# Kernel tuning notes

Measured on AMD Instinct MI355X. Metric: run time of the kernel, lower is better.

The kernel has to match this reference:

```python
import jax, jax.numpy as jnp
import numpy as np

NUM_HEADS = 16


def setup_inputs() -> dict:
    key = jax.random.key(0)
    ks = jax.random.split(key, 7)
    B, S, D = 2, 2048, 1024
    scale = 1.0 / np.sqrt(D)
    return {
        "queries": jax.random.normal(ks[0], (B, S, D), jnp.float32),
        "keys": jax.random.normal(ks[1], (B, S, D), jnp.float32),
        "values": jax.random.normal(ks[2], (B, S, D), jnp.float32),
        "Wq": jax.random.normal(ks[3], (D, D), jnp.float32) * scale,
        "Wk": jax.random.normal(ks[4], (D, D), jnp.float32) * scale,
        "Wv": jax.random.normal(ks[5], (D, D), jnp.float32) * scale,
        "Wo": jax.random.normal(ks[6], (D, D), jnp.float32) * scale,
    }


def _split_heads(x, h):
    # [B, S, D] -> [B, h, S, D/h]
    B, S, D = x.shape
    return x.reshape(B, S, h, D // h).transpose(0, 2, 1, 3)


def reference(queries, keys, values, Wq, Wk, Wv, Wo):
    h = NUM_HEADS
    q = _split_heads(queries @ Wq, h)  # [B, h, S, dh]
    k = _split_heads(keys @ Wk, h)
    v = _split_heads(values @ Wv, h)
    dh = q.shape[-1]
    scores = jnp.einsum("bhqd,bhkd->bhqk", q, k) / jnp.sqrt(jnp.float32(dh))
    attn = jax.nn.softmax(scores, axis=-1)
    y = jnp.einsum("bhqk,bhkd->bhqd", attn, v)  # [B, h, S, dh]
    B, _, S, _ = y.shape
    y = y.transpose(0, 2, 1, 3).reshape(B, S, h * dh)
    return y @ Wo
```

## Files before the change

kernel.cpp:

```cpp
#include <hip/hip_runtime.h>
#include <hip/hip_bf16.h>


typedef __attribute__((ext_vector_type(8))) short bf16x8;
typedef __attribute__((ext_vector_type(4))) float f32x4;
typedef __attribute__((ext_vector_type(16))) float f32x16;
typedef __attribute__((ext_vector_type(4))) unsigned int u32x4;

#define QSCALE 0.18033688011112042f

__device__ __forceinline__ unsigned short f2b(float f) {
    unsigned int u = __float_as_uint(f);
    u += 0x7FFFu + ((u >> 16) & 1u);
    return (unsigned short)(u >> 16);
}

__device__ __forceinline__ unsigned cvt_pk_bf16(float lo, float hi) {
    unsigned r;
    asm("v_cvt_pk_bf16_f32 %0, %1, %2" : "=v"(r) : "v"(lo), "v"(hi));
    return r;
}

__device__ __forceinline__ void gld_lds16(const void* g, void* l) {
    __builtin_amdgcn_global_load_lds(
        (const __attribute__((address_space(1))) unsigned int*)g,
        (__attribute__((address_space(3))) unsigned int*)l, 16, 0, 0);
}

__global__ __launch_bounds__(256) void f32_to_bf16_3(
    const float* __restrict__ i0, const float* __restrict__ i1, const float* __restrict__ i2,
    unsigned short* __restrict__ o0, unsigned short* __restrict__ o1, unsigned short* __restrict__ o2)
{
    const int z = blockIdx.y;
    const float* in = z == 0 ? i0 : (z == 1 ? i1 : i2);
    unsigned short* out = z == 0 ? o0 : (z == 1 ? o1 : o2);
    int i = blockIdx.x * 256 + threadIdx.x;
    float4 v = ((const float4*)in)[i];
    ushort4 o;
    o.x = f2b(v.x); o.y = f2b(v.y); o.z = f2b(v.z); o.w = f2b(v.w);
    ((ushort4*)out)[i] = o;
}

__global__ __launch_bounds__(256) void transpose_w4(
    const float* __restrict__ W0, const float* __restrict__ W1,
    const float* __restrict__ W2, const float* __restrict__ W3,
    unsigned short* __restrict__ O0, unsigned short* __restrict__ O1,
    unsigned short* __restrict__ O2, unsigned short* __restrict__ O3)
{
    __shared__ unsigned short tile[32][33];
    const int z = blockIdx.z;
    const float* in = z == 0 ? W0 : z == 1 ? W1 : z == 2 ? W2 : W3;
    unsigned short* out = z == 0 ? O0 : z == 1 ? O1 : z == 2 ? O2 : O3;
    const int c0 = blockIdx.x * 32, r0 = blockIdx.y * 32;
    const int tx = threadIdx.x, ty = threadIdx.y;
#pragma unroll
    for (int i = 0; i < 4; ++i)
        tile[ty + i * 8][tx] = f2b(in[(size_t)(r0 + ty + i * 8) * 1024 + c0 + tx]);
    __syncthreads();
#pragma unroll
    for (int i = 0; i < 4; ++i)
        out[(size_t)(c0 + ty + i * 8) * 1024 + r0 + tx] = tile[tx][ty + i * 8];
}

__device__ __forceinline__ void vpack_store(unsigned short* Vp, int gr, int gc,
                                            const f32x4& a)
{
    int bq = gr >> 11, kvg = gr & 2047, kvt = kvg >> 6;
    int h = gc >> 6, d = gc & 63;
    size_t img = ((size_t)(bq * 16 + h) * 32 + kvt) * 4096;
    int kvb = kvg & 63;
    int T = kvb >> 5, g = (kvb >> 3) & 3, hib = (kvb >> 2) & 1;
    int kstep = 2 * T + (g >> 1);
    int dt = d >> 5, ln31 = d & 31;
    size_t addr = img + dt * 2048 + kstep * 512 + hib * 256 + ln31 * 8 + (g & 1) * 4;
    uint2 w;
    w.x = cvt_pk_bf16(a[0], a[1]);
    w.y = cvt_pk_bf16(a[2], a[3]);
    *(uint2*)(Vp + addr) = w;
}

__device__ __forceinline__ int lds_fragaddr(int slot, int mat, int half, int row,
                                            int ks, int lg)
{
    int c8s = lg ^ ((row >> 1) & 3);
    return slot * 32768 + mat * 16384 + half * 8192 +
           (((row >> 4) * 2 + ks) * 512) + (row & 15) * 32 + c8s * 8;
}

__global__ __launch_bounds__(512, 2) void gemm256(
    const unsigned short* __restrict__ A0, const unsigned short* __restrict__ A1,
    const unsigned short* __restrict__ A2,
    const unsigned short* __restrict__ B0, const unsigned short* __restrict__ B1,
    const unsigned short* __restrict__ B2,
    unsigned short* __restrict__ Cq,
    unsigned short* __restrict__ Ckrm,
    unsigned short* __restrict__ Cv)
{
    __shared__ unsigned short lds[65536];
    const int tid = threadIdx.x;
    const int wid = tid >> 6, ln = tid & 15, lg = (tid & 63) >> 4;
    const int wr = wid >> 2, wc = wid & 3;
    const int z = blockIdx.z;
    const unsigned short* A = (z == 0) ? A0 : (z == 1) ? A1 : A2;
    const unsigned short* Bt = (z == 0) ? B0 : (z == 1) ? B1 : B2;
    const int m0 = blockIdx.y * 256, n0 = blockIdx.x * 256;

    f32x4 acc[8][4];
#pragma unroll
    for (int m = 0; m < 8; ++m)
#pragma unroll
        for (int n = 0; n < 4; ++n) acc[m][n] = {};

    const unsigned short* srcA[2][2];
    const unsigned short* srcB[2][2];
#pragma unroll
    for (int j = 0; j < 2; ++j) {
        const int ci = tid + j * 512;
        const int s = ci >> 6, r16 = (ci >> 2) & 15, c8 = ci & 3;
        const int c8s = c8 ^ ((r16 >> 1) & 3);
        const int rih = (s >> 1) * 16 + r16;
        const int colc = (s & 1) * 4 + c8s;
#pragma unroll
        for (int half = 0; half < 2; ++half) {
            srcA[j][half] = A + (size_t)(m0 + half * 128 + rih) * 1024 + colc * 8;
            srcB[j][half] = Bt + (size_t)(n0 + half * 128 + rih) * 1024 + colc * 8;
        }
    }

    auto stage = [&](int slot, int k0) {
#pragma unroll
        for (int j = 0; j < 2; ++j) {
            const int ci = tid + j * 512;
#pragma unroll
            for (int half = 0; half < 2; ++half) {
                gld_lds16(srcA[j][half] + k0,
                          &lds[slot * 32768 + half * 8192 + ci * 8]);
                gld_lds16(srcB[j][half] + k0,
                          &lds[slot * 32768 + 16384 + half * 8192 + ci * 8]);
            }
        }
    };

    stage(0, 0);
    __syncthreads();

    for (int t = 0; t < 16; ++t) {
        const int slot = t & 1;
        if (t < 15) stage(slot ^ 1, (t + 1) * 64);

#pragma unroll
        for (int qd = 0; qd < 4; ++qd) {
            const int mh = qd >> 1, nh = qd & 1;
            bf16x8 af[4][2], bfr[2][2];
#pragma unroll
            for (int mm = 0; mm < 4; ++mm)
#pragma unroll
                for (int ks = 0; ks < 2; ++ks)
                    af[mm][ks] = *(const bf16x8*)&lds[
                        lds_fragaddr(slot, 0, wr, (mh * 4 + mm) * 16 + ln, ks, lg)];
#pragma unroll
            for (int nn = 0; nn < 2; ++nn)
#pragma unroll
                for (int ks = 0; ks < 2; ++ks)
                    bfr[nn][ks] = *(const bf16x8*)&lds[
                        lds_fragaddr(slot, 1, wc >> 1,
                                     (wc & 1) * 64 + (nh * 2 + nn) * 16 + ln, ks, lg)];
            __builtin_amdgcn_s_setprio(1);
#pragma unroll
            for (int mm = 0; mm < 4; ++mm)
#pragma unroll
                for (int nn = 0; nn < 2; ++nn)
#pragma unroll
                    for (int ks = 0; ks < 2; ++ks)
                        acc[mh * 4 + mm][nh * 2 + nn] =
                            __builtin_amdgcn_mfma_f32_16x16x32_bf16(
                                af[mm][ks], bfr[nn][ks],
                                acc[mh * 4 + mm][nh * 2 + nn], 0, 0, 0);
            __builtin_amdgcn_s_setprio(0);
        }
        __syncthreads();
    }

#pragma unroll
    for (int m = 0; m < 8; ++m)
#pragma unroll
        for (int n = 0; n < 4; ++n) {
            const int gr = m0 + wr * 128 + m * 16 + lg * 4;
            const int gc = n0 + wc * 64 + n * 16 + ln;
            if (z == 0) {
#pragma unroll
                for (int r = 0; r < 4; ++r)
                    Cq[(size_t)(gr + r) * 1024 + gc] = f2b(acc[m][n][r] * QSCALE);
            } else if (z == 1) {
#pragma unroll
                for (int r = 0; r < 4; ++r)
                    Ckrm[(size_t)(gr + r) * 1024 + gc] = f2b(acc[m][n][r]);
            } else {
                vpack_store(Cv, gr, gc, acc[m][n]);
            }
        }
}

template <int BN, int MODE>
__global__ __launch_bounds__(256) void gemm_bt(
    const unsigned short* __restrict__ A0,
    const unsigned short* __restrict__ B0,
    void* __restrict__ Cq)
{
    constexpr int K = 1024, N = 1024;
    constexpr int NB = BN / 32;
    __shared__ unsigned short lds_a[2][128 * 32];
    __shared__ unsigned short lds_b[2][BN * 32];
    const int tid = threadIdx.x;
    const int wid = tid >> 6, ln = tid & 15, lg = (tid & 63) >> 4;
    const unsigned short* A = A0;
    const unsigned short* Bt = B0;
    const int m0 = blockIdx.y * 128, n0 = blockIdx.x * BN;
    const int wr = wid >> 1, wc = wid & 1;

    f32x4 acc[4][NB];
#pragma unroll
    for (int m = 0; m < 4; ++m)
#pragma unroll
        for (int n = 0; n < NB; ++n) acc[m][n] = {};

    const unsigned short* ga = A + (size_t)(m0 + (tid >> 2)) * K + (tid & 3) * 8;
    const unsigned short* gb = Bt + (size_t)(n0 + (tid >> 2)) * K + (tid & 3) * 8;

    auto stage = [&](int buf, int k0) {
        gld_lds16(ga + k0, &lds_a[buf][wid * 512]);
        gld_lds16(ga + k0 + 64 * K, &lds_a[buf][wid * 512 + 2048]);
        gld_lds16(gb + k0, &lds_b[buf][wid * 512]);
        if constexpr (BN == 128) gld_lds16(gb + k0 + 64 * K, &lds_b[buf][wid * 512 + 2048]);
    };

    stage(0, 0);
    __syncthreads();

    for (int k0 = 0; k0 < K; k0 += 32) {
        const int buf = (k0 >> 5) & 1;
        if (k0 + 32 < K) stage(buf ^ 1, k0 + 32);

        bf16x8 af[4], bfr[NB];
#pragma unroll
        for (int m = 0; m < 4; ++m)
            af[m] = *(const bf16x8*)&lds_a[buf][(wr * 64 + m * 16 + ln) * 32 + lg * 8];
#pragma unroll
        for (int n = 0; n < NB; ++n)
            bfr[n] = *(const bf16x8*)&lds_b[buf][(wc * (BN / 2) + n * 16 + ln) * 32 + lg * 8];
#pragma unroll
        for (int m = 0; m < 4; ++m)
#pragma unroll
            for (int n = 0; n < NB; ++n)
                acc[m][n] = __builtin_amdgcn_mfma_f32_16x16x32_bf16(af[m], bfr[n], acc[m][n], 0, 0, 0);
        __syncthreads();
    }

    const int gcb = n0 + wc * (BN / 2) + ln;
    const int grb = m0 + wr * 64 + lg * 4;
    float* C = (float*)Cq;
#pragma unroll
    for (int m = 0; m < 4; ++m)
#pragma unroll
        for (int n = 0; n < NB; ++n)
#pragma unroll
            for (int r = 0; r < 4; ++r)
                C[(size_t)(grb + m * 16 + r) * N + gcb + n * 16] = acc[m][n][r];
}

__global__ __launch_bounds__(256) void k_repack(
    const unsigned short* __restrict__ Krm, unsigned short* __restrict__ Kp)
{
    const int kvt = blockIdx.x, bh = blockIdx.y;
    const int bq = bh >> 4, h = bh & 15;
    const int tid = threadIdx.x;
    const int kvr = tid & 31, hib = (tid >> 5) & 1, ks = (tid >> 6) & 3;
    const size_t img = ((size_t)bh * 32 + kvt) * 4096;
#pragma unroll
    for (int T = 0; T < 2; ++T) {
        const int row = bq * 2048 + kvt * 64 + T * 32 + kvr;
        bf16x8 v = *(const bf16x8*)&Krm[(size_t)row * 1024 + h * 64 + ks * 16 + hib * 8];
        *(bf16x8*)&Kp[img + T * 2048 + ks * 512 + hib * 256 + kvr * 8] = v;
    }
}

__global__ __launch_bounds__(256) void attn_kernel(
    const unsigned short* __restrict__ Qp,
    const unsigned short* __restrict__ Kpack,
    const unsigned short* __restrict__ Vpack,
    unsigned short* __restrict__ Y)
{
    __shared__ unsigned short lds_k[2][4096];
    __shared__ unsigned short lds_v[2][4096];
    const int tid = threadIdx.x;
    const int wid = tid >> 6, lane = tid & 63;
    const int q31 = lane & 31, hi = lane >> 5;

    const int logical = (blockIdx.x & 7) * 64 + (blockIdx.x >> 3);
    const int bx = logical & 15, bh = logical >> 4;
    const int b = bh >> 4, h = bh & 15;
    const int tok0 = b * 2048;
    const int qw = bx * 128 + wid * 32;

    const unsigned short* qrow = Qp + (size_t)(tok0 + qw + q31) * 1024 + h * 64 + hi * 8;
    bf16x8 qf[4];
#pragma unroll
    for (int ks = 0; ks < 4; ++ks) qf[ks] = *(const bf16x8*)(qrow + ks * 16);

    const unsigned short* gk = Kpack + (size_t)bh * (32 * 4096);
    const unsigned short* gv = Vpack + (size_t)bh * (32 * 4096);

    float l_run = 0.f;
    f32x16 o[2] = {{}, {}};

    auto stage = [&](int buf, int kvt) {
#pragma unroll
        for (int j = 0; j < 2; ++j) {
            int seg = wid * 2 + j;
            gld_lds16(gk + (size_t)kvt * 4096 + seg * 512 + lane * 8, &lds_k[buf][seg * 512]);
            gld_lds16(gv + (size_t)kvt * 4096 + seg * 512 + lane * 8, &lds_v[buf][seg * 512]);
        }
    };

    stage(0, 0);
    __syncthreads();

    for (int kvt = 0; kvt < 32; ++kvt) {
        const int buf = kvt & 1;
        if (kvt < 31) stage(buf ^ 1, kvt + 1);

        f32x16 st[2];
#pragma unroll
        for (int T = 0; T < 2; ++T) {
            f32x16 zacc = {};
#pragma unroll
            for (int ks = 0; ks < 4; ++ks) {
                bf16x8 ka = *(const bf16x8*)&lds_k[buf][T * 2048 + ks * 512 + lane * 8];
                zacc = __builtin_amdgcn_mfma_f32_32x32x16_bf16(ka, qf[ks], zacc, 0, 0, 0);
            }
            st[T] = zacc;
        }

        float rs = 0.f;
        unsigned pk[2][8];
#pragma unroll
        for (int T = 0; T < 2; ++T)
#pragma unroll
            for (int g = 0; g < 4; ++g) {
                float p0 = __builtin_amdgcn_exp2f(st[T][g * 4 + 0]);
                float p1 = __builtin_amdgcn_exp2f(st[T][g * 4 + 1]);
                float p2 = __builtin_amdgcn_exp2f(st[T][g * 4 + 2]);
                float p3 = __builtin_amdgcn_exp2f(st[T][g * 4 + 3]);
                rs += (p0 + p1) + (p2 + p3);
                pk[T][g * 2 + 0] = cvt_pk_bf16(p0, p1);
                pk[T][g * 2 + 1] = cvt_pk_bf16(p2, p3);
            }
        rs += __shfl_xor(rs, 32);
        l_run += rs;

#pragma unroll
        for (int dt = 0; dt < 2; ++dt)
#pragma unroll
            for (int kstep = 0; kstep < 4; ++kstep) {
                bf16x8 va = *(const bf16x8*)&lds_v[buf][dt * 2048 + kstep * 512 + lane * 8];
                u32x4 w = {pk[kstep >> 1][4 * (kstep & 1) + 0], pk[kstep >> 1][4 * (kstep & 1) + 1],
                           pk[kstep >> 1][4 * (kstep & 1) + 2], pk[kstep >> 1][4 * (kstep & 1) + 3]};
                o[dt] = __builtin_amdgcn_mfma_f32_32x32x16_bf16(
                    va, __builtin_bit_cast(bf16x8, w), o[dt], 0, 0, 0);
            }
        __syncthreads();
    }

    const float inv = __builtin_amdgcn_rcpf(l_run);
    unsigned short* yout = Y + (size_t)(tok0 + qw + q31) * 1024 + h * 64 + hi * 4;
#pragma unroll
    for (int dt = 0; dt < 2; ++dt)
#pragma unroll
        for (int g = 0; g < 4; ++g) {
            uint2 w;
            w.x = cvt_pk_bf16(o[dt][g * 4 + 0] * inv, o[dt][g * 4 + 1] * inv);
            w.y = cvt_pk_bf16(o[dt][g * 4 + 2] * inv, o[dt][g * 4 + 3] * inv);
            *(uint2*)(yout + dt * 32 + g * 8) = w;
        }
}

extern "C" void kernel_launch(void* const* d_in, const int* in_sizes, int n_in,
                              void* d_out, int out_size, void* d_ws, size_t ws_size,
                              hipStream_t stream)
{
    const float* q_f = (const float*)d_in[0];
    const float* k_f = (const float*)d_in[1];
    const float* v_f = (const float*)d_in[2];
    const float* Wq  = (const float*)d_in[3];
    const float* Wk  = (const float*)d_in[4];
    const float* Wv  = (const float*)d_in[5];
    const float* Wo  = (const float*)d_in[6];
    float* out = (float*)d_out;

    const size_t X = (size_t)4096 * 1024;
    const size_t W = (size_t)1024 * 1024;
    unsigned short* ws  = (unsigned short*)d_ws;
    unsigned short* qb  = ws;
    unsigned short* kb  = qb + X;
    unsigned short* vb  = kb + X;
    unsigned short* wqt = vb + X;
    unsigned short* wkt = wqt + W;
    unsigned short* wvt = wkt + W;
    unsigned short* wot = wvt + W;
    unsigned short* Qp  = wot + W;
    unsigned short* Kpk = Qp + X;
    unsigned short* Vpk = Kpk + X;
    unsigned short* Yb  = Vpk + X;
    unsigned short* Krm = Yb;

    f32_to_bf16_3<<<dim3(4096, 3), 256, 0, stream>>>(q_f, k_f, v_f, qb, kb, vb);
    transpose_w4<<<dim3(32, 32, 4), dim3(32, 8), 0, stream>>>(Wq, Wk, Wv, Wo,
                                                              wqt, wkt, wvt, wot);

    gemm256<<<dim3(4, 16, 3), 512, 0, stream>>>(qb, kb, vb, wqt, wkt, wvt,
                                                Qp, Krm, Vpk);
    k_repack<<<dim3(32, 32), 256, 0, stream>>>(Krm, Kpk);

    attn_kernel<<<512, 256, 0, stream>>>(Qp, Kpk, Vpk, Yb);

    gemm_bt<64, 0><<<dim3(16, 32), 256, 0, stream>>>(Yb, wot, out);
}
```

Measured before the change: 221.8 us.

## Fuse K repack into projection GEMM epilogue and halve attention block size

The K projection GEMM now writes directly into the packed per-head tile layout used by attention, which removes the separate k_repack kernel and its extra read and write of the K matrix. The attention kernel goes from 256 to 128 threads per block and from 512 to 1024 blocks, each covering 64 queries, so each wave stages twice as many K/V segments. The fused store writes scalar bf16 values with a strided pattern, which may coalesce worse than the old row-major writes. Smaller blocks give more blocks for the scheduler but reuse each staged K/V tile across fewer query waves.

After: 231.0 us. 1.04x slower.

```diff
diff --git a/kernel.cpp b/kernel.cpp
--- a/kernel.cpp
+++ b/kernel.cpp
@@ -79,6 +79,20 @@
     *(uint2*)(Vp + addr) = w;
 }
 
+__device__ __forceinline__ void kpack_store(unsigned short* Kp, int gr0, int gc,
+                                            const f32x4& a)
+{
+    int bq = gr0 >> 11, kvg = gr0 & 2047, kvt = kvg >> 6;
+    int h = gc >> 6, d = gc & 63;
+    size_t img = ((size_t)(bq * 16 + h) * 32 + kvt) * 4096;
+    int ks = d >> 4, hib = (d >> 3) & 1, i = d & 7;
+    int kvb = kvg & 63, T = kvb >> 5;
+    size_t base = img + T * 2048 + ks * 512 + hib * 256 + i;
+#pragma unroll
+    for (int r = 0; r < 4; ++r)
+        Kp[base + ((kvb & 31) + r) * 8] = f2b(a[r]);
+}
+
 __device__ __forceinline__ int lds_fragaddr(int slot, int mat, int half, int row,
                                             int ks, int lg)
 {
@@ -93,7 +107,7 @@
     const unsigned short* __restrict__ B0, const unsigned short* __restrict__ B1,
     const unsigned short* __restrict__ B2,
     unsigned short* __restrict__ Cq,
-    unsigned short* __restrict__ Ckrm,
+    unsigned short* __restrict__ Ck,
     unsigned short* __restrict__ Cv)
 {
     __shared__ unsigned short lds[65536];
@@ -192,9 +206,7 @@
                 for (int r = 0; r < 4; ++r)
                     Cq[(size_t)(gr + r) * 1024 + gc] = f2b(acc[m][n][r] * QSCALE);
             } else if (z == 1) {
-#pragma unroll
-                for (int r = 0; r < 4; ++r)
-                    Ckrm[(size_t)(gr + r) * 1024 + gc] = f2b(acc[m][n][r]);
+                kpack_store(Ck, gr, gc, acc[m][n]);
             } else {
                 vpack_store(Cv, gr, gc, acc[m][n]);
             }
@@ -268,23 +280,7 @@
                 C[(size_t)(grb + m * 16 + r) * N + gcb + n * 16] = acc[m][n][r];
 }
 
-__global__ __launch_bounds__(256) void k_repack(
-    const unsigned short* __restrict__ Krm, unsigned short* __restrict__ Kp)
-{
-    const int kvt = blockIdx.x, bh = blockIdx.y;
-    const int bq = bh >> 4, h = bh & 15;
-    const int tid = threadIdx.x;
-    const int kvr = tid & 31, hib = (tid >> 5) & 1, ks = (tid >> 6) & 3;
-    const size_t img = ((size_t)bh * 32 + kvt) * 4096;
-#pragma unroll
-    for (int T = 0; T < 2; ++T) {
-        const int row = bq * 2048 + kvt * 64 + T * 32 + kvr;
-        bf16x8 v = *(const bf16x8*)&Krm[(size_t)row * 1024 + h * 64 + ks * 16 + hib * 8];
-        *(bf16x8*)&Kp[img + T * 2048 + ks * 512 + hib * 256 + kvr * 8] = v;
-    }
-}
-
-__global__ __launch_bounds__(256) void attn_kernel(
+__global__ __launch_bounds__(128) void attn_kernel(
     const unsigned short* __restrict__ Qp,
     const unsigned short* __restrict__ Kpack,
     const unsigned short* __restrict__ Vpack,
@@ -296,11 +292,11 @@
     const int wid = tid >> 6, lane = tid & 63;
     const int q31 = lane & 31, hi = lane >> 5;
 
-    const int logical = (blockIdx.x & 7) * 64 + (blockIdx.x >> 3);
-    const int bx = logical & 15, bh = logical >> 4;
+    const int logical = (blockIdx.x & 7) * 128 + (blockIdx.x >> 3);
+    const int bx = logical & 31, bh = logical >> 5;
     const int b = bh >> 4, h = bh & 15;
     const int tok0 = b * 2048;
-    const int qw = bx * 128 + wid * 32;
+    const int qw = bx * 64 + wid * 32;
 
     const unsigned short* qrow = Qp + (size_t)(tok0 + qw + q31) * 1024 + h * 64 + hi * 8;
     bf16x8 qf[4];
@@ -315,8 +311,8 @@
 
     auto stage = [&](int buf, int kvt) {
 #pragma unroll
-        for (int j = 0; j < 2; ++j) {
-            int seg = wid * 2 + j;
+        for (int j = 0; j < 4; ++j) {
+            int seg = wid * 4 + j;
             gld_lds16(gk + (size_t)kvt * 4096 + seg * 512 + lane * 8, &lds_k[buf][seg * 512]);
             gld_lds16(gv + (size_t)kvt * 4096 + seg * 512 + lane * 8, &lds_v[buf][seg * 512]);
         }
@@ -411,17 +407,15 @@
     unsigned short* Kpk = Qp + X;
     unsigned short* Vpk = Kpk + X;
     unsigned short* Yb  = Vpk + X;
-    unsigned short* Krm = Yb;
 
     f32_to_bf16_3<<<dim3(4096, 3), 256, 0, stream>>>(q_f, k_f, v_f, qb, kb, vb);
     transpose_w4<<<dim3(32, 32, 4), dim3(32, 8), 0, stream>>>(Wq, Wk, Wv, Wo,
                                                               wqt, wkt, wvt, wot);
 
     gemm256<<<dim3(4, 16, 3), 512, 0, stream>>>(qb, kb, vb, wqt, wkt, wvt,
-                                                Qp, Krm, Vpk);
-    k_repack<<<dim3(32, 32), 256, 0, stream>>>(Krm, Kpk);
-
-    attn_kernel<<<512, 256, 0, stream>>>(Qp, Kpk, Vpk, Yb);
+                                                Qp, Kpk, Vpk);
+
+    attn_kernel<<<1024, 128, 0, stream>>>(Qp, Kpk, Vpk, Yb);
 
     gemm_bt<64, 0><<<dim3(16, 32), 256, 0, stream>>>(Yb, wot, out);
 }
```
